# Kernel tuning notes

Measured on AMD Instinct MI355X. Metric: run time of the kernel, lower is better.

Reference implementation:

```python
import jax, jax.numpy as jnp
import numpy as np
import math

D_MODEL = 512
N_HEADS = 8
MAX_SPAN = 512
SPAN_LOSS_COEF = 2e-4
NEG_INF = -1.0e9
R_SIZE = 4.0


def soft_span_mask(span, max_span, seq_len):
    # span: (H,) clamped span fractions
    i_idx = jnp.arange(seq_len, dtype=span.dtype)[:, None]
    j_idx = jnp.arange(seq_len, dtype=span.dtype)[None, :]
    dist = i_idx - j_idx                                  # (T, T)
    eff_span = (span * max_span)[:, None, None]           # (H, 1, 1)
    x = eff_span - dist[None, :, :]                       # (H, T, T)
    R = jnp.clip((x + 1.0) / R_SIZE, 0.0, 1.0)
    causal_ok = dist[None, :, :] >= 0
    log_R = jnp.maximum(jnp.log(R + 1e-10), NEG_INF)
    return jnp.where(causal_ok & (R > 0), log_R, NEG_INF)  # (H, T, T)


def setup_inputs() -> dict:
    key = jax.random.key(0)
    ks = jax.random.split(key, 6)
    B, T, D = 4, 2048, D_MODEL
    w_scale = 0.02
    return {
        "x": jax.random.normal(ks[0], (B, T, D), dtype=jnp.float32),
        "wq": jax.random.normal(ks[1], (D, D), dtype=jnp.float32) * w_scale,
        "wk": jax.random.normal(ks[2], (D, D), dtype=jnp.float32) * w_scale,
        "wv": jax.random.normal(ks[3], (D, D), dtype=jnp.float32) * w_scale,
        "wo": jax.random.normal(ks[4], (D, D), dtype=jnp.float32) * w_scale,
        "span_params": jax.random.uniform(ks[5], (N_HEADS,), dtype=jnp.float32),
    }


def reference(x, wq, wk, wv, wo, span_params):
    B, T, D = x.shape
    H = N_HEADS
    d_h = D // H

    clamped_span = jnp.clip(span_params, 0.0, 1.0)

    # nn.Linear(bias=False): y = x @ W.T
    Q = (x @ wq.T).reshape(B, T, H, d_h).transpose(0, 2, 1, 3)  # (B,H,T,dh)
    K = (x @ wk.T).reshape(B, T, H, d_h).transpose(0, 2, 1, 3)
    V = (x @ wv.T).reshape(B, T, H, d_h).transpose(0, 2, 1, 3)

    scale = 1.0 / math.sqrt(d_h)
    scores = jnp.einsum("bhqd,bhkd->bhqk", Q, K) * scale        # (B,H,T,T)
    scores = scores + soft_span_mask(clamped_span, MAX_SPAN, T)[None]

    weights = jax.nn.softmax(scores, axis=-1)
    out = jnp.einsum("bhqk,bhkd->bhqd", weights, V)             # (B,H,T,dh)
    out = out.transpose(0, 2, 1, 3).reshape(B, T, D)
    output = out @ wo.T

    span_loss = SPAN_LOSS_COEF * clamped_span.mean()
    return output, span_loss
```

## Files before the change

kernel.cpp:

```cpp
#include <hip/hip_runtime.h>
#include <math.h>

#define T_SEQ   2048
#define DMODEL  512
#define NHEADS  8
#define DH      64
#define NEG_INF -1.0e9f

typedef __attribute__((ext_vector_type(8))) short short8;
typedef __attribute__((ext_vector_type(4))) float f32x4;
typedef unsigned int u32;
typedef unsigned short u16;

__device__ __forceinline__ u16 f2bf(float f) {
    union { float f; u32 u; } w; w.f = f;
    return (u16)((w.u + 0x8000u) >> 16);
}

__device__ __forceinline__ void async_load16(const u16* g, u16* l) {
    __builtin_amdgcn_global_load_lds(
        (const __attribute__((address_space(1))) u32*)(const void*)g,
        (__attribute__((address_space(3))) u32*)(void*)l, 16, 0, 0);
}

__global__ void cast_all(const float* __restrict__ x,  const float* __restrict__ wq,
                         const float* __restrict__ wk, const float* __restrict__ wv,
                         const float* __restrict__ wo, const float* __restrict__ sp,
                         u16* __restrict__ xb,  u16* __restrict__ wqb,
                         u16* __restrict__ wkb, u16* __restrict__ wvb,
                         u16* __restrict__ wob, float* __restrict__ loss_out)
{
    const int bid = blockIdx.x;
    const float* src; u16* dst; int i;
    if (bid < 4096) { src = x; dst = xb; i = bid * 256 + threadIdx.x; }
    else {
        const int wsel = (bid - 4096) >> 8;
        src = (wsel == 0) ? wq : (wsel == 1) ? wk : (wsel == 2) ? wv : wo;
        dst = (wsel == 0) ? wqb : (wsel == 1) ? wkb : (wsel == 2) ? wvb : wob;
        i = ((bid - 4096) & 255) * 256 + threadIdx.x;
    }
    float4 v = ((const float4*)src)[i];
    ushort4 o;
    o.x = f2bf(v.x); o.y = f2bf(v.y); o.z = f2bf(v.z); o.w = f2bf(v.w);
    ((ushort4*)dst)[i] = o;
    if (bid == 5119 && threadIdx.x == 0) {
        float s = 0.0f;
        for (int h = 0; h < NHEADS; ++h)
            s += fminf(fmaxf(sp[h], 0.0f), 1.0f);
        loss_out[0] = 2e-4f * (s * 0.125f);
    }
}

__global__ __launch_bounds__(256)
void gemm_bf16(const u16* __restrict__ A,
               const u16* __restrict__ W0, const u16* __restrict__ W1,
               const u16* __restrict__ W2,
               u16* __restrict__ Cb0, u16* __restrict__ Cb1,
               u16* __restrict__ Cb2,
               float* __restrict__ Cf, int scatter)
{
    constexpr int K = 512, BK = 64;
    const u16* W  = (blockIdx.z == 0) ? W0 : (blockIdx.z == 1) ? W1 : W2;
    u16*       Cb = (blockIdx.z == 0) ? Cb0 : (blockIdx.z == 1) ? Cb1 : Cb2;

    __shared__ __align__(16) u16 smem[16384];
    u16* As = smem;
    u16* Bs = smem + 8192;

    const int t    = threadIdx.x;
    const int lane = t & 63;
    const int wave = t >> 6;
    const int wm   = wave >> 1, wn = wave & 1;
    const int m0   = blockIdx.x * 128, n0 = blockIdx.y * 128;

    const int srow = t >> 3;
    const int kb   = (t & 7) ^ (srow & 7);
    const u16* gA = A + (size_t)(m0 + srow) * K + kb * 8;
    const u16* gW = W + (size_t)(n0 + srow) * K + kb * 8;

    const int rA = wm * 64 + (lane & 15);
    const int rB = wn * 64 + (lane & 15);
    const int kq = lane >> 4;
    const int offA0 = rA * BK + ((kq      ^ (rA & 7)) * 8);
    const int offA1 = rA * BK + (((4 + kq) ^ (rA & 7)) * 8);
    const int offB0 = rB * BK + ((kq      ^ (rB & 7)) * 8);
    const int offB1 = rB * BK + (((4 + kq) ^ (rB & 7)) * 8);

    f32x4 acc[4][4];
#pragma unroll
    for (int it = 0; it < 4; ++it)
#pragma unroll
        for (int jt = 0; jt < 4; ++jt) acc[it][jt] = (f32x4)0.0f;

    for (int k0 = 0; k0 < K; k0 += BK) {
        __syncthreads();
#pragma unroll
        for (int i = 0; i < 4; ++i) {
            async_load16(gA + k0 + i * (32 * K), As + t * 8 + i * 2048);
            async_load16(gW + k0 + i * (32 * K), Bs + t * 8 + i * 2048);
        }
        __syncthreads();

        short8 af[4][2], bfr[4][2];
#pragma unroll
        for (int it = 0; it < 4; ++it) {
            af[it][0]  = *(const short8*)(As + offA0 + it * 16 * BK);
            af[it][1]  = *(const short8*)(As + offA1 + it * 16 * BK);
            bfr[it][0] = *(const short8*)(Bs + offB0 + it * 16 * BK);
            bfr[it][1] = *(const short8*)(Bs + offB1 + it * 16 * BK);
        }
#pragma unroll
        for (int it = 0; it < 4; ++it)
#pragma unroll
            for (int jt = 0; jt < 4; ++jt) {
                acc[it][jt] = __builtin_amdgcn_mfma_f32_16x16x32_bf16(
                    af[it][0], bfr[jt][0], acc[it][jt], 0, 0, 0);
                acc[it][jt] = __builtin_amdgcn_mfma_f32_16x16x32_bf16(
                    af[it][1], bfr[jt][1], acc[it][jt], 0, 0, 0);
            }
    }

    const int r0 = (lane >> 4) * 4;
    const int cl = lane & 15;

    if (scatter) {
        constexpr int P = 136;
#pragma unroll
        for (int rnd = 0; rnd < 2; ++rnd) {
            __syncthreads();
#pragma unroll
            for (int s = 0; s < 2; ++s) {
                const int it = rnd * 2 + s;
                const int lrow = wm * 32 + s * 16 + r0;
#pragma unroll
                for (int jt = 0; jt < 4; ++jt) {
                    const int cc = wn * 64 + jt * 16 + cl;
#pragma unroll
                    for (int r = 0; r < 4; ++r)
                        smem[(lrow + r) * P + cc] = f2bf(acc[it][jt][r]);
                }
            }
            __syncthreads();
            const int lrow2 = t >> 2;
            const int h2    = (t >> 1) & 1;
            const int dhalf = t & 1;
            const int grow  = m0 + (lrow2 >> 5) * 64 + rnd * 32 + (lrow2 & 31);
            const int b     = grow >> 11, tt = grow & 2047;
            const int h     = (n0 >> 6) + h2;
            u16* dst = Cb + ((size_t)((b * NHEADS + h) * T_SEQ + tt)) * DH + dhalf * 32;
            const u16* srcl = smem + lrow2 * P + h2 * 64 + dhalf * 32;
#pragma unroll
            for (int i = 0; i < 4; ++i)
                ((uint4*)dst)[i] = *(const uint4*)(srcl + i * 8);
        }
    } else {
#pragma unroll
        for (int it = 0; it < 4; ++it) {
#pragma unroll
            for (int r = 0; r < 4; ++r) {
                const int row = m0 + wm * 64 + it * 16 + r0 + r;
#pragma unroll
                for (int jt = 0; jt < 4; ++jt) {
                    const int col = n0 + wn * 64 + jt * 16 + cl;
                    Cf[(size_t)row * DMODEL + col] = acc[it][jt][r];
                }
            }
        }
    }
}

__global__ __launch_bounds__(256)
void transpose_v(const u16* __restrict__ V, u16* __restrict__ Vt)
{
    __shared__ u16 tile[64][72];
    const int bh = blockIdx.y;
    const int j0 = blockIdx.x * 64;
    const u16* src = V + (size_t)bh * (T_SEQ * DH) + (size_t)j0 * DH;
    u16* dst = Vt + (size_t)bh * (T_SEQ * DH) + j0;
    const int t = threadIdx.x;
    const int jr = t >> 2, c0 = (t & 3) * 16;
    uint4 a = *(const uint4*)(src + (size_t)jr * DH + c0);
    uint4 b = *(const uint4*)(src + (size_t)jr * DH + c0 + 8);
    *(uint4*)&tile[jr][c0]     = a;
    *(uint4*)&tile[jr][c0 + 8] = b;
    __syncthreads();
    const int d = t >> 2, jc = (t & 3) * 16;
    union { uint4 v; u16 s[8]; } pa, pb;
#pragma unroll
    for (int i = 0; i < 8; ++i) pa.s[i] = tile[jc + i][d];
#pragma unroll
    for (int i = 0; i < 8; ++i) pb.s[i] = tile[jc + 8 + i][d];
    *(uint4*)(dst + (size_t)d * T_SEQ + jc)     = pa.v;
    *(uint4*)(dst + (size_t)d * T_SEQ + jc + 8) = pb.v;
}

__global__ __launch_bounds__(128)
void attn_mfma(const u16* __restrict__ Q, const u16* __restrict__ K,
               const u16* __restrict__ Vt, const float* __restrict__ span_params,
               u16* __restrict__ out)
{
    __shared__ __align__(16) u16 Ks[64 * 64];
    __shared__ __align__(16) u16 Vs[64 * 64];
    __shared__ __align__(16) u16 Ps[2][16 * 76];

    const int tid  = threadIdx.x;
    const int lane = tid & 63;
    const int w    = tid >> 6;
    const int nl   = lane & 15;
    const int quad = lane >> 4;
    const int bh   = blockIdx.y;
    const int b    = bh >> 3, h = bh & 7;
    const int i0   = blockIdx.x * 32;
    const int q0   = i0 + w * 16;

    const u16* Qh = Q  + (size_t)bh * (T_SEQ * DH);
    const u16* Kh = K  + (size_t)bh * (T_SEQ * DH);
    const u16* Vh = Vt + (size_t)bh * (DH * T_SEQ);

    float span = span_params[h];
    span = fminf(fmaxf(span, 0.0f), 1.0f);
    const float eff_span = span * 512.0f;
    const int wspan = (int)(eff_span + 1.0f) + 1;

    short8 qf0 = *(const short8*)(Qh + (size_t)(q0 + nl) * DH + quad * 8);
    short8 qf1 = *(const short8*)(Qh + (size_t)(q0 + nl) * DH + 32 + quad * 8);

    const int srow = tid >> 3;
    const int sg   = (tid & 7) ^ (srow & 7);
    const u16* gK = Kh + (size_t)srow * DH + sg * 8;
    const u16* gV = Vh + (size_t)srow * T_SEQ + sg * 8;

    f32x4 o[4];
    float m_r[4], l_r[4];
#pragma unroll
    for (int d = 0; d < 4; ++d) o[d] = (f32x4)0.0f;
#pragma unroll
    for (int r = 0; r < 4; ++r) { m_r[r] = -1.0e30f; l_r[r] = 0.0f; }

    int j_lo = i0 - wspan;
    if (j_lo < 0) j_lo = 0;
    j_lo &= ~63;

    for (int j0 = j_lo; j0 <= i0 + 31; j0 += 64) {
        __syncthreads();
#pragma unroll
        for (int i = 0; i < 4; ++i) {
            async_load16(gK + (size_t)(j0 + i * 16) * DH, Ks + tid * 8 + i * 1024);
            async_load16(gV + j0 + (size_t)(i * 16) * T_SEQ, Vs + tid * 8 + i * 1024);
        }
        __syncthreads();

        f32x4 s[4];
        bool any[4];
#pragma unroll
        for (int n = 0; n < 4; ++n) {
            const int jn = j0 + n * 16;
            any[n] = (jn <= q0 + 15) &&
                     ((float)(q0 - jn - 15) < eff_span + 1.0f);
            s[n] = (f32x4)0.0f;
            if (any[n]) {
                const int row = n * 16 + nl;
                const u16* kp = Ks + row * 64;
                short8 b0 = *(const short8*)(kp + ((quad ^ (row & 7)) * 8));
                short8 b1 = *(const short8*)(kp + (((4 + quad) ^ (row & 7)) * 8));
                s[n] = __builtin_amdgcn_mfma_f32_16x16x32_bf16(qf0, b0, s[n], 0, 0, 0);
                s[n] = __builtin_amdgcn_mfma_f32_16x16x32_bf16(qf1, b1, s[n], 0, 0, 0);
            }
        }

        float tmax[4] = {-1.0e30f, -1.0e30f, -1.0e30f, -1.0e30f};
#pragma unroll
        for (int n = 0; n < 4; ++n) {
            if (!any[n]) continue;
            const int jn = j0 + n * 16;
            const bool causal_b = (jn + 15 > q0);
            const bool span_b   = ((float)(q0 + 15 - jn) > eff_span - 3.0f);
            if (!causal_b && !span_b) {
#pragma unroll
                for (int r = 0; r < 4; ++r) {
                    const float sv = s[n][r] * 0.125f;
                    s[n][r] = sv;
                    tmax[r] = fmaxf(tmax[r], sv);
                }
            } else if (!span_b) {
#pragma unroll
                for (int r = 0; r < 4; ++r) {
                    const int dist = (q0 + quad * 4 + r) - (jn + nl);
                    const float sv = (dist >= 0) ? s[n][r] * 0.125f : NEG_INF;
                    s[n][r] = sv;
                    tmax[r] = fmaxf(tmax[r], sv);
                }
            } else {
#pragma unroll
                for (int r = 0; r < 4; ++r) {
                    const int dist = (q0 + quad * 4 + r) - (jn + nl);
                    float sv = NEG_INF;
                    if (dist >= 0) {
                        float xv = eff_span - (float)dist;
                        float R  = fminf(fmaxf((xv + 1.0f) * 0.25f, 0.0f), 1.0f);
                        if (R > 0.0f)
                            sv = s[n][r] * 0.125f +
                                 ((R < 1.0f) ? __logf(R + 1e-10f) : 0.0f);
                    }
                    s[n][r] = sv;
                    tmax[r] = fmaxf(tmax[r], sv);
                }
            }
        }

        float alpha[4];
#pragma unroll
        for (int r = 0; r < 4; ++r) {
            float t = tmax[r];
            t = fmaxf(t, __shfl_xor(t, 1));
            t = fmaxf(t, __shfl_xor(t, 2));
            t = fmaxf(t, __shfl_xor(t, 4));
            t = fmaxf(t, __shfl_xor(t, 8));
            const float m_new = fmaxf(m_r[r], t);
            alpha[r] = __expf(m_r[r] - m_new);
            m_r[r] = m_new;
        }

        float psum[4] = {0.0f, 0.0f, 0.0f, 0.0f};
#pragma unroll
        for (int n = 0; n < 4; ++n) {
            if (any[n]) {
#pragma unroll
                for (int r = 0; r < 4; ++r) {
                    const float pv = __expf(s[n][r] - m_r[r]);
                    psum[r] += pv;
                    Ps[w][(quad * 4 + r) * 76 + n * 16 + nl] = f2bf(pv);
                }
            } else {
#pragma unroll
                for (int r = 0; r < 4; ++r)
                    Ps[w][(quad * 4 + r) * 76 + n * 16 + nl] = 0;
            }
        }
#pragma unroll
        for (int r = 0; r < 4; ++r) {
            float ps = psum[r];
            ps += __shfl_xor(ps, 1);
            ps += __shfl_xor(ps, 2);
            ps += __shfl_xor(ps, 4);
            ps += __shfl_xor(ps, 8);
            l_r[r] = l_r[r] * alpha[r] + ps;
#pragma unroll
            for (int d = 0; d < 4; ++d) o[d][r] *= alpha[r];
        }

        const bool kf0 = any[0] | any[1];
        const bool kf1 = any[2] | any[3];
        const u16* pb = Ps[w] + nl * 76;
        short8 a0 = *(const short8*)(pb + quad * 8);
        short8 a1 = *(const short8*)(pb + 32 + quad * 8);
#pragma unroll
        for (int d = 0; d < 4; ++d) {
            const int vrow = d * 16 + nl;
            const u16* vp = Vs + vrow * 64;
            if (kf0) {
                short8 vb0 = *(const short8*)(vp + ((quad ^ (vrow & 7)) * 8));
                o[d] = __builtin_amdgcn_mfma_f32_16x16x32_bf16(a0, vb0, o[d], 0, 0, 0);
            }
            if (kf1) {
                short8 vb1 = *(const short8*)(vp + (((4 + quad) ^ (vrow & 7)) * 8));
                o[d] = __builtin_amdgcn_mfma_f32_16x16x32_bf16(a1, vb1, o[d], 0, 0, 0);
            }
        }
    }

#pragma unroll
    for (int r = 0; r < 4; ++r) {
        const int qg = q0 + quad * 4 + r;
        const float inv_l = 1.0f / l_r[r];
        u16* op = out + (size_t)(b * T_SEQ + qg) * DMODEL + h * 64;
#pragma unroll
        for (int d = 0; d < 4; ++d)
            op[d * 16 + nl] = f2bf(o[d][r] * inv_l);
    }
}

extern "C" void kernel_launch(void* const* d_in, const int* in_sizes, int n_in,
                              void* d_out, int out_size, void* d_ws, size_t ws_size,
                              hipStream_t stream)
{
    (void)in_sizes; (void)n_in; (void)out_size; (void)ws_size;
    const float* x  = (const float*)d_in[0];
    const float* wq = (const float*)d_in[1];
    const float* wk = (const float*)d_in[2];
    const float* wv = (const float*)d_in[3];
    const float* wo = (const float*)d_in[4];
    const float* sp = (const float*)d_in[5];
    float* out = (float*)d_out;

    const size_t elems = (size_t)4 * T_SEQ * DMODEL;
    u16* xb  = (u16*)d_ws;
    u16* Qb  = xb  + elems;
    u16* Kb  = Qb  + elems;
    u16* Vb  = Kb  + elems;
    u16* Vtb = Vb  + elems;
    u16* Ab  = Vtb + elems;
    u16* wqb = Ab  + elems;
    u16* wkb = wqb + 262144;
    u16* wvb = wkb + 262144;
    u16* wob = wvb + 262144;

    cast_all<<<5120, 256, 0, stream>>>(x, wq, wk, wv, wo, sp,
                                       xb, wqb, wkb, wvb, wob, out + elems);
    gemm_bf16<<<dim3(64, 4, 3), 256, 0, stream>>>(
        xb, wqb, wkb, wvb, Qb, Kb, Vb, nullptr, 1);
    transpose_v<<<dim3(32, 32), 256, 0, stream>>>(Vb, Vtb);
    attn_mfma<<<dim3(64, 32), 128, 0, stream>>>(Qb, Kb, Vtb, sp, Ab);
    gemm_bf16<<<dim3(64, 4, 1), 256, 0, stream>>>(
        Ab, wob, wob, wob, nullptr, nullptr, nullptr, out, 0);
}
```

Measured before the change: 161.7 us.

## Double-buffer K/V tiles in attention, widen blocks to 4 waves, remap grid

The attention kernel now uses 256-thread blocks covering 64 queries. K/V tiles are double-buffered in LDS, and the next tile is prefetched asynchronously with explicit vmcnt waits and raw barriers, so global loads overlap with compute. The grid is flattened to 1D with a custom mapping that interleaves heads and batches, probably for cache locality and load balance, and s_setprio is raised around the MFMA sections. This doubles LDS use and raises the exact-count vmcnt and barrier-ordering risk, while halving the number of blocks.

```diff
diff --git a/kernel.cpp b/kernel.cpp
--- a/kernel.cpp
+++ b/kernel.cpp
@@ -21,6 +21,12 @@
     __builtin_amdgcn_global_load_lds(
         (const __attribute__((address_space(1))) u32*)(const void*)g,
         (__attribute__((address_space(3))) u32*)(void*)l, 16, 0, 0);
+}
+
+__device__ __forceinline__ void barrier_raw() {
+    __builtin_amdgcn_sched_barrier(0);
+    asm volatile("s_barrier" ::: "memory");
+    __builtin_amdgcn_sched_barrier(0);
 }
 
 __global__ void cast_all(const float* __restrict__ x,  const float* __restrict__ wq,
@@ -194,24 +200,28 @@
     *(uint4*)(dst + (size_t)d * T_SEQ + jc + 8) = pb.v;
 }
 
-__global__ __launch_bounds__(128)
+__global__ __launch_bounds__(256)
 void attn_mfma(const u16* __restrict__ Q, const u16* __restrict__ K,
                const u16* __restrict__ Vt, const float* __restrict__ span_params,
                u16* __restrict__ out)
 {
-    __shared__ __align__(16) u16 Ks[64 * 64];
-    __shared__ __align__(16) u16 Vs[64 * 64];
-    __shared__ __align__(16) u16 Ps[2][16 * 76];
+    __shared__ __align__(16) u16 Ks[2][64 * 64];
+    __shared__ __align__(16) u16 Vs[2][64 * 64];
+    __shared__ __align__(16) u16 Ps[4][16 * 76];
 
     const int tid  = threadIdx.x;
     const int lane = tid & 63;
     const int w    = tid >> 6;
     const int nl   = lane & 15;
     const int quad = lane >> 4;
-    const int bh   = blockIdx.y;
-    const int b    = bh >> 3, h = bh & 7;
-    const int i0   = blockIdx.x * 32;
-    const int q0   = i0 + w * 16;
+
+    const int l  = blockIdx.x;
+    const int h  = ((l >> 8) * 2 + (l & 1)) & 7;
+    const int b  = (l >> 1) & 3;
+    const int qb = (l >> 3) & 31;
+    const int bh = b * 8 + h;
+    const int i0 = qb * 64;
+    const int q0 = i0 + w * 16;
 
     const u16* Qh = Q  + (size_t)bh * (T_SEQ * DH);
     const u16* Kh = K  + (size_t)bh * (T_SEQ * DH);
@@ -230,6 +240,13 @@
     const u16* gK = Kh + (size_t)srow * DH + sg * 8;
     const u16* gV = Vh + (size_t)srow * T_SEQ + sg * 8;
 
+#define ATTN_ISSUE(bi, jj) do {                                              \
+        async_load16(gK + (size_t)(jj) * DH,            Ks[bi] + tid * 8);        \
+        async_load16(gK + (size_t)((jj) + 32) * DH,     Ks[bi] + tid * 8 + 2048); \
+        async_load16(gV + (jj),                         Vs[bi] + tid * 8);        \
+        async_load16(gV + (size_t)32 * T_SEQ + (jj),    Vs[bi] + tid * 8 + 2048); \
+    } while (0)
+
     f32x4 o[4];
     float m_r[4], l_r[4];
 #pragma unroll
@@ -240,18 +257,28 @@
     int j_lo = i0 - wspan;
     if (j_lo < 0) j_lo = 0;
     j_lo &= ~63;
-
-    for (int j0 = j_lo; j0 <= i0 + 31; j0 += 64) {
-        __syncthreads();
-#pragma unroll
-        for (int i = 0; i < 4; ++i) {
-            async_load16(gK + (size_t)(j0 + i * 16) * DH, Ks + tid * 8 + i * 1024);
-            async_load16(gV + j0 + (size_t)(i * 16) * T_SEQ, Vs + tid * 8 + i * 1024);
-        }
-        __syncthreads();
+    const int nt = ((i0 - j_lo) >> 6) + 1;
+
+    ATTN_ISSUE(0, j_lo);
+    int buf = 0;
+
+    for (int t = 0; t < nt; ++t) {
+        const int j0 = j_lo + (t << 6);
+
+        if (t + 1 < nt) {
+            ATTN_ISSUE(buf ^ 1, j0 + 64);
+            asm volatile("s_waitcnt vmcnt(4)" ::: "memory");
+        } else {
+            asm volatile("s_waitcnt vmcnt(0)" ::: "memory");
+        }
+        barrier_raw();
+
+        const u16* Kb = Ks[buf];
+        const u16* Vb = Vs[buf];
 
         f32x4 s[4];
         bool any[4];
+        __builtin_amdgcn_s_setprio(1);
 #pragma unroll
         for (int n = 0; n < 4; ++n) {
             const int jn = j0 + n * 16;
@@ -260,13 +287,14 @@
             s[n] = (f32x4)0.0f;
             if (any[n]) {
                 const int row = n * 16 + nl;
-                const u16* kp = Ks + row * 64;
+                const u16* kp = Kb + row * 64;
                 short8 b0 = *(const short8*)(kp + ((quad ^ (row & 7)) * 8));
                 short8 b1 = *(const short8*)(kp + (((4 + quad) ^ (row & 7)) * 8));
                 s[n] = __builtin_amdgcn_mfma_f32_16x16x32_bf16(qf0, b0, s[n], 0, 0, 0);
                 s[n] = __builtin_amdgcn_mfma_f32_16x16x32_bf16(qf1, b1, s[n], 0, 0, 0);
             }
         }
+        __builtin_amdgcn_s_setprio(0);
 
         float tmax[4] = {-1.0e30f, -1.0e30f, -1.0e30f, -1.0e30f};
 #pragma unroll
@@ -311,12 +339,12 @@
         float alpha[4];
 #pragma unroll
         for (int r = 0; r < 4; ++r) {
-            float t = tmax[r];
-            t = fmaxf(t, __shfl_xor(t, 1));
-            t = fmaxf(t, __shfl_xor(t, 2));
-            t = fmaxf(t, __shfl_xor(t, 4));
-            t = fmaxf(t, __shfl_xor(t, 8));
-            const float m_new = fmaxf(m_r[r], t);
+            float t2 = tmax[r];
+            t2 = fmaxf(t2, __shfl_xor(t2, 1));
+            t2 = fmaxf(t2, __shfl_xor(t2, 2));
+            t2 = fmaxf(t2, __shfl_xor(t2, 4));
+            t2 = fmaxf(t2, __shfl_xor(t2, 8));
+            const float m_new = fmaxf(m_r[r], t2);
             alpha[r] = __expf(m_r[r] - m_new);
             m_r[r] = m_new;
         }
@@ -354,10 +382,11 @@
         const u16* pb = Ps[w] + nl * 76;
         short8 a0 = *(const short8*)(pb + quad * 8);
         short8 a1 = *(const short8*)(pb + 32 + quad * 8);
+        __builtin_amdgcn_s_setprio(1);
 #pragma unroll
         for (int d = 0; d < 4; ++d) {
             const int vrow = d * 16 + nl;
-            const u16* vp = Vs + vrow * 64;
+            const u16* vp = Vb + vrow * 64;
             if (kf0) {
                 short8 vb0 = *(const short8*)(vp + ((quad ^ (vrow & 7)) * 8));
                 o[d] = __builtin_amdgcn_mfma_f32_16x16x32_bf16(a0, vb0, o[d], 0, 0, 0);
@@ -367,7 +396,12 @@
                 o[d] = __builtin_amdgcn_mfma_f32_16x16x32_bf16(a1, vb1, o[d], 0, 0, 0);
             }
         }
-    }
+        __builtin_amdgcn_s_setprio(0);
+
+        barrier_raw();
+        buf ^= 1;
+    }
+#undef ATTN_ISSUE
 
 #pragma unroll
     for (int r = 0; r < 4; ++r) {
@@ -410,7 +444,7 @@
     gemm_bf16<<<dim3(64, 4, 3), 256, 0, stream>>>(
         xb, wqb, wkb, wvb, Qb, Kb, Vb, nullptr, 1);
     transpose_v<<<dim3(32, 32), 256, 0, stream>>>(Vb, Vtb);
-    attn_mfma<<<dim3(64, 32), 128, 0, stream>>>(Qb, Kb, Vtb, sp, Ab);
+    attn_mfma<<<dim3(1024), 256, 0, stream>>>(Qb, Kb, Vtb, sp, Ab);
     gemm_bf16<<<dim3(64, 4, 1), 256, 0, stream>>>(
         Ab, wob, wob, wob, nullptr, nullptr, nullptr, out, 0);
 }
```

After: 167.5 us. 3.6% more time.

## Load K/V fragments directly from global, reorder blocks heavy-first, use exp2 softmax

Applied to the files above, without the earlier changes.

Drops the shared-memory staging of K and V tiles and the two block barriers per iteration; each wave now reads its MFMA operands straight from global memory, relying on L1/L2. The grid is flattened and ordered so blocks with the most key tiles (late query blocks) launch first, and the launch bounds request higher occupancy. Softmax is rewritten in base 2 with the scale folded into a log2e-scaled constant, and s_setprio is raised around the MFMA sections. The trade-off is that K/V reuse across the two waves no longer happens through LDS, so global and cache traffic per block rises.

```diff
diff --git a/kernel.cpp b/kernel.cpp
--- a/kernel.cpp
+++ b/kernel.cpp
@@ -194,13 +194,11 @@
     *(uint4*)(dst + (size_t)d * T_SEQ + jc + 8) = pb.v;
 }
 
-__global__ __launch_bounds__(128)
+__global__ __launch_bounds__(128, 4)
 void attn_mfma(const u16* __restrict__ Q, const u16* __restrict__ K,
                const u16* __restrict__ Vt, const float* __restrict__ span_params,
                u16* __restrict__ out)
 {
-    __shared__ __align__(16) u16 Ks[64 * 64];
-    __shared__ __align__(16) u16 Vs[64 * 64];
     __shared__ __align__(16) u16 Ps[2][16 * 76];
 
     const int tid  = threadIdx.x;
@@ -208,10 +206,14 @@
     const int w    = tid >> 6;
     const int nl   = lane & 15;
     const int quad = lane >> 4;
-    const int bh   = blockIdx.y;
-    const int b    = bh >> 3, h = bh & 7;
-    const int i0   = blockIdx.x * 32;
-    const int q0   = i0 + w * 16;
+
+    const int l  = blockIdx.x;
+    const int bh = l & 31;
+    const int h  = bh & 7;
+    const int b  = bh >> 3;
+    const int qb = 63 - (l >> 5);
+    const int i0 = qb * 32;
+    const int q0 = i0 + w * 16;
 
     const u16* Qh = Q  + (size_t)bh * (T_SEQ * DH);
     const u16* Kh = K  + (size_t)bh * (T_SEQ * DH);
@@ -222,13 +224,10 @@
     const float eff_span = span * 512.0f;
     const int wspan = (int)(eff_span + 1.0f) + 1;
 
+    const float SCL = 0.125f * 1.44269504f;
+
     short8 qf0 = *(const short8*)(Qh + (size_t)(q0 + nl) * DH + quad * 8);
     short8 qf1 = *(const short8*)(Qh + (size_t)(q0 + nl) * DH + 32 + quad * 8);
-
-    const int srow = tid >> 3;
-    const int sg   = (tid & 7) ^ (srow & 7);
-    const u16* gK = Kh + (size_t)srow * DH + sg * 8;
-    const u16* gV = Vh + (size_t)srow * T_SEQ + sg * 8;
 
     f32x4 o[4];
     float m_r[4], l_r[4];
@@ -241,17 +240,13 @@
     if (j_lo < 0) j_lo = 0;
     j_lo &= ~63;
 
+    const u16* Kp0 = Kh + (size_t)nl * DH + quad * 8;
+    const u16* Vp0 = Vh + (size_t)nl * T_SEQ + quad * 8;
+
     for (int j0 = j_lo; j0 <= i0 + 31; j0 += 64) {
-        __syncthreads();
-#pragma unroll
-        for (int i = 0; i < 4; ++i) {
-            async_load16(gK + (size_t)(j0 + i * 16) * DH, Ks + tid * 8 + i * 1024);
-            async_load16(gV + j0 + (size_t)(i * 16) * T_SEQ, Vs + tid * 8 + i * 1024);
-        }
-        __syncthreads();
-
         f32x4 s[4];
         bool any[4];
+        __builtin_amdgcn_s_setprio(1);
 #pragma unroll
         for (int n = 0; n < 4; ++n) {
             const int jn = j0 + n * 16;
@@ -259,14 +254,14 @@
                      ((float)(q0 - jn - 15) < eff_span + 1.0f);
             s[n] = (f32x4)0.0f;
             if (any[n]) {
-                const int row = n * 16 + nl;
-                const u16* kp = Ks + row * 64;
-                short8 b0 = *(const short8*)(kp + ((quad ^ (row & 7)) * 8));
-                short8 b1 = *(const short8*)(kp + (((4 + quad) ^ (row & 7)) * 8));
+                const u16* kp = Kp0 + (size_t)jn * DH;
+                short8 b0 = *(const short8*)(kp);
+                short8 b1 = *(const short8*)(kp + 32);
                 s[n] = __builtin_amdgcn_mfma_f32_16x16x32_bf16(qf0, b0, s[n], 0, 0, 0);
                 s[n] = __builtin_amdgcn_mfma_f32_16x16x32_bf16(qf1, b1, s[n], 0, 0, 0);
             }
         }
+        __builtin_amdgcn_s_setprio(0);
 
         float tmax[4] = {-1.0e30f, -1.0e30f, -1.0e30f, -1.0e30f};
 #pragma unroll
@@ -278,7 +273,7 @@
             if (!causal_b && !span_b) {
 #pragma unroll
                 for (int r = 0; r < 4; ++r) {
-                    const float sv = s[n][r] * 0.125f;
+                    const float sv = s[n][r] * SCL;
                     s[n][r] = sv;
                     tmax[r] = fmaxf(tmax[r], sv);
                 }
@@ -286,7 +281,7 @@
 #pragma unroll
                 for (int r = 0; r < 4; ++r) {
                     const int dist = (q0 + quad * 4 + r) - (jn + nl);
-                    const float sv = (dist >= 0) ? s[n][r] * 0.125f : NEG_INF;
+                    const float sv = (dist >= 0) ? s[n][r] * SCL : NEG_INF;
                     s[n][r] = sv;
                     tmax[r] = fmaxf(tmax[r], sv);
                 }
@@ -299,8 +294,8 @@
                         float xv = eff_span - (float)dist;
                         float R  = fminf(fmaxf((xv + 1.0f) * 0.25f, 0.0f), 1.0f);
                         if (R > 0.0f)
-                            sv = s[n][r] * 0.125f +
-                                 ((R < 1.0f) ? __logf(R + 1e-10f) : 0.0f);
+                            sv = s[n][r] * SCL +
+                                 ((R < 1.0f) ? __log2f(R + 1e-10f) : 0.0f);
                     }
                     s[n][r] = sv;
                     tmax[r] = fmaxf(tmax[r], sv);
@@ -311,13 +306,13 @@
         float alpha[4];
 #pragma unroll
         for (int r = 0; r < 4; ++r) {
-            float t = tmax[r];
-            t = fmaxf(t, __shfl_xor(t, 1));
-            t = fmaxf(t, __shfl_xor(t, 2));
-            t = fmaxf(t, __shfl_xor(t, 4));
-            t = fmaxf(t, __shfl_xor(t, 8));
-            const float m_new = fmaxf(m_r[r], t);
-            alpha[r] = __expf(m_r[r] - m_new);
+            float t2 = tmax[r];
+            t2 = fmaxf(t2, __shfl_xor(t2, 1));
+            t2 = fmaxf(t2, __shfl_xor(t2, 2));
+            t2 = fmaxf(t2, __shfl_xor(t2, 4));
+            t2 = fmaxf(t2, __shfl_xor(t2, 8));
+            const float m_new = fmaxf(m_r[r], t2);
+            alpha[r] = exp2f(m_r[r] - m_new);
             m_r[r] = m_new;
         }
 
@@ -327,7 +322,7 @@
             if (any[n]) {
 #pragma unroll
                 for (int r = 0; r < 4; ++r) {
-                    const float pv = __expf(s[n][r] - m_r[r]);
+                    const float pv = exp2f(s[n][r] - m_r[r]);
                     psum[r] += pv;
                     Ps[w][(quad * 4 + r) * 76 + n * 16 + nl] = f2bf(pv);
                 }
@@ -354,19 +349,20 @@
         const u16* pb = Ps[w] + nl * 76;
         short8 a0 = *(const short8*)(pb + quad * 8);
         short8 a1 = *(const short8*)(pb + 32 + quad * 8);
+        __builtin_amdgcn_s_setprio(1);
 #pragma unroll
         for (int d = 0; d < 4; ++d) {
-            const int vrow = d * 16 + nl;
-            const u16* vp = Vs + vrow * 64;
+            const u16* vp = Vp0 + (size_t)(d * 16) * T_SEQ + j0;
             if (kf0) {
-                short8 vb0 = *(const short8*)(vp + ((quad ^ (vrow & 7)) * 8));
+                short8 vb0 = *(const short8*)(vp);
                 o[d] = __builtin_amdgcn_mfma_f32_16x16x32_bf16(a0, vb0, o[d], 0, 0, 0);
             }
             if (kf1) {
-                short8 vb1 = *(const short8*)(vp + (((4 + quad) ^ (vrow & 7)) * 8));
+                short8 vb1 = *(const short8*)(vp + 32);
                 o[d] = __builtin_amdgcn_mfma_f32_16x16x32_bf16(a1, vb1, o[d], 0, 0, 0);
             }
         }
+        __builtin_amdgcn_s_setprio(0);
     }
 
 #pragma unroll
@@ -410,7 +406,7 @@
     gemm_bf16<<<dim3(64, 4, 3), 256, 0, stream>>>(
         xb, wqb, wkb, wvb, Qb, Kb, Vb, nullptr, 1);
     transpose_v<<<dim3(32, 32), 256, 0, stream>>>(Vb, Vtb);
-    attn_mfma<<<dim3(64, 32), 128, 0, stream>>>(Qb, Kb, Vtb, sp, Ab);
+    attn_mfma<<<dim3(2048), 128, 0, stream>>>(Qb, Kb, Vtb, sp, Ab);
     gemm_bf16<<<dim3(64, 4, 1), 256, 0, stream>>>(
         Ab, wob, wob, wob, nullptr, nullptr, nullptr, out, 0);
 }
```

Result: slower. 173.7 us (+7.4%).
